# Kernel tuning notes

Hardware: AMD Instinct MI355X
Metric: run time of the kernel (lower is better)

The kernel has to match this reference:

```python
import jax, jax.numpy as jnp
import numpy as np

N, E = 50000, 640000
FEAT, EMB, HID, B = 128, 128, 512, 32


def setup_inputs() -> dict:
    key = jax.random.key(0)
    ks = jax.random.split(key, 12)
    def w(k, shape, fan_in):
        return jax.random.normal(k, shape, dtype=jnp.float32) / np.sqrt(fan_in)
    return {
        "x": jax.random.normal(ks[0], (N, FEAT), dtype=jnp.float32),
        "edge_index": jax.random.randint(ks[1], (2, E), 0, N, dtype=jnp.int64),
        "last_hidden": jax.random.normal(ks[2], (1, B, HID), dtype=jnp.float32),
        "W1_rel": w(ks[3], (FEAT, EMB), FEAT),
        "W1_root": w(ks[4], (FEAT, EMB), FEAT),
        "b1": jnp.zeros((EMB,), dtype=jnp.float32),
        "W2_rel": w(ks[5], (EMB, EMB), EMB),
        "W2_root": w(ks[6], (EMB, EMB), EMB),
        "b2": jnp.zeros((EMB,), dtype=jnp.float32),
        "Wp": w(ks[7], (HID, EMB), HID),
        "bp": jnp.zeros((EMB,), dtype=jnp.float32),
    }


def _rgcn(h, src, dst, W_rel, W_root, b):
    # transform-then-gather (N < E so cheaper): messages along edges src->dst
    msg = (h @ W_rel)[src]                                   # [E, emb]
    agg = jax.ops.segment_sum(msg, dst, num_segments=N)      # [N, emb]
    deg = jax.ops.segment_sum(jnp.ones((E,), h.dtype), dst, num_segments=N)
    agg = agg / jnp.maximum(deg, 1.0)[:, None]               # mean aggregation (PyG RGCNConv default)
    return agg + h @ W_root + b


def reference(x, edge_index, last_hidden, W1_rel, W1_root, b1, W2_rel, W2_root, b2, Wp, bp):
    src, dst = edge_index[0], edge_index[1]
    h = jax.nn.relu(_rgcn(x, src, dst, W1_rel, W1_root, b1))   # [N, emb]
    h = jax.nn.relu(_rgcn(h, src, dst, W2_rel, W2_root, b2))   # [N, emb]
    message_embed = (last_hidden @ Wp + bp)[0]                 # squeeze(0) -> [B, emb]
    scores = h @ message_embed.T                               # [N, B]
    return jax.nn.log_softmax(scores, axis=0)
```

## Files before the change

kernel.cpp:

```cpp
#include <hip/hip_runtime.h>
#include <hip/hip_bf16.h>

#define N_NODES 50000
#define N_EDGES 640000
#define DUMMY   N_NODES
#define CAP     56

typedef __attribute__((ext_vector_type(8))) short short8;
typedef __attribute__((ext_vector_type(4))) float floatx4;

__device__ __forceinline__ float bf2f(unsigned short u) {
    return __uint_as_float(((unsigned int)u) << 16);
}
__device__ __forceinline__ unsigned short f2bf(float x) {
    unsigned int u = __float_as_uint(x);
    u = (u + 0x7fffu + ((u >> 16) & 1u)) >> 16;
    return (unsigned short)u;
}
__device__ __forceinline__ unsigned char f2f8(float x) {
    int pk = __builtin_amdgcn_cvt_pk_fp8_f32(x, x, 0, false);
    return (unsigned char)(pk & 0xff);
}
__device__ __forceinline__ unsigned int pk4_fp8(float x0, float x1, float x2, float x3) {
    int v = __builtin_amdgcn_cvt_pk_fp8_f32(x0, x1, 0, false);
    v = __builtin_amdgcn_cvt_pk_fp8_f32(x2, x3, v, true);
    return (unsigned int)v;
}
__device__ __forceinline__ unsigned int pk2_bf16(float lo, float hi) {
    return (unsigned int)f2bf(lo) | ((unsigned int)f2bf(hi) << 16);
}

__global__ void __launch_bounds__(256) prep_k(const float* __restrict__ W0,
                                              const float* __restrict__ W1,
                                              const float* __restrict__ W2,
                                              const float* __restrict__ W3,
                                              unsigned short* __restrict__ T0,
                                              unsigned short* __restrict__ T1,
                                              unsigned short* __restrict__ T2,
                                              unsigned short* __restrict__ T3,
                                              int* __restrict__ cnt,
                                              const float* __restrict__ lh,
                                              const float* __restrict__ Wp,
                                              const float* __restrict__ bp,
                                              unsigned short* __restrict__ meb,
                                              unsigned short* __restrict__ ssrc,
                                              unsigned char* __restrict__ tbf,
                                              const int* __restrict__ src,
                                              const int* __restrict__ dst) {
    int b = blockIdx.x, tid = threadIdx.x;
    bool is_hist;
    int idx;
    if (b < 546) { is_hist = ((b & 1) == 0); idx = b >> 1; }
    else         { is_hist = true;            idx = 273 + (b - 546); }
    if (is_hist) {
        int e = idx * 256 + tid;
        int d = dst[e];
        int r = atomicAdd(&cnt[d], 1);
        if (r < CAP) ssrc[d * CAP + r] = (unsigned short)src[e];
        return;
    }
    int s = idx;
    if (s < 256) {
        int i2 = s * 256 + tid;
        int w = i2 >> 14;
        int r = i2 & 16383;
        int n = r >> 7, k = r & 127;
        const float* W = (w == 0) ? W0 : (w == 1) ? W1 : (w == 2) ? W2 : W3;
        unsigned short* T = (w == 0) ? T0 : (w == 1) ? T1 : (w == 2) ? T2 : T3;
        T[r] = f2bf(W[k * 128 + n]);
    } else if (s < 272) {
        int o = (s - 256) * 256 + tid;
        int i = o >> 7, c = o & 127;
        float acc = bp[c];
        const float4* lr = (const float4*)(lh + i * 512);
        #pragma unroll 4
        for (int k4 = 0; k4 < 128; k4++) {
            float4 v = lr[k4];
            acc += v.x * Wp[(4 * k4 + 0) * 128 + c] + v.y * Wp[(4 * k4 + 1) * 128 + c]
                 + v.z * Wp[(4 * k4 + 2) * 128 + c] + v.w * Wp[(4 * k4 + 3) * 128 + c];
        }
        meb[o] = f2bf(acc);
    } else {
        if (tid < 32) ((unsigned int*)(tbf + (size_t)DUMMY * 128))[tid] = 0;
    }
}

#define EPI_LD 132
template <bool AF32>
__device__ __forceinline__ void gemm_dual_lds32(int bid, int tid,
                                                const void* __restrict__ Ain,
                                                const unsigned short* __restrict__ BtRel,
                                                const unsigned short* __restrict__ BtRoot,
                                                unsigned char* __restrict__ Trel,
                                                unsigned short* __restrict__ Rootb,
                                                int M, char* __restrict__ pool) {
    int wid = tid >> 6, lane = tid & 63;
    int m = lane & 15, g = lane >> 4;
    int r0 = bid * 32;
    if constexpr (AF32) {
        const float* A = (const float*)Ain;
        #pragma unroll
        for (int j = 0; j < 2; j++) {
            int k = j * 256 + tid;
            int row = k >> 4;
            int grow = r0 + row; grow = (grow < M) ? grow : (M - 1);
            const float* p = A + (size_t)grow * 128 + (k & 15) * 8;
            float4 v0 = *(const float4*)p;
            float4 v1 = *(const float4*)(p + 4);
            short8 t8;
            t8[0] = (short)f2bf(v0.x); t8[1] = (short)f2bf(v0.y);
            t8[2] = (short)f2bf(v0.z); t8[3] = (short)f2bf(v0.w);
            t8[4] = (short)f2bf(v1.x); t8[5] = (short)f2bf(v1.y);
            t8[6] = (short)f2bf(v1.z); t8[7] = (short)f2bf(v1.w);
            *(short8*)(pool + ((k * 16) ^ ((row & 7) << 4))) = t8;
        }
    } else {
        const unsigned short* A = (const unsigned short*)Ain;
        #pragma unroll
        for (int j = 0; j < 2; j++) {
            int k = j * 256 + tid;
            int row = k >> 4;
            int grow = r0 + row; grow = (grow < M) ? grow : (M - 1);
            short8 v = *(const short8*)(A + (size_t)grow * 128 + (k & 15) * 8);
            *(short8*)(pool + ((k * 16) ^ ((row & 7) << 4))) = v;
        }
    }
    #pragma unroll
    for (int j = 0; j < 8; j++) {
        int k = j * 256 + tid;
        int row = k >> 4;
        short8 v = *(const short8*)(BtRel + (size_t)k * 8);
        *(short8*)(pool + 8192 + ((k * 16) ^ ((row & 7) << 4))) = v;
    }
    __syncthreads();
    int lrow = (wid >> 1) * 16 + m;
    int asw = (lrow & 7) << 4, abase = lrow * 256;
    short8 a[4];
    #pragma unroll
    for (int kt = 0; kt < 4; kt++)
        a[kt] = *(const short8*)(pool + ((abase + kt * 64 + g * 16) ^ asw));
    int browbase = (wid & 1) * 64;
    floatx4 accR[4], accO[4];
    #pragma unroll
    for (int ct = 0; ct < 4; ct++) {
        accR[ct] = (floatx4)(0.f);
        int brow = browbase + ct * 16 + m;
        int bbase = brow * 256, bsw = (brow & 7) << 4;
        #pragma unroll
        for (int kt = 0; kt < 4; kt++) {
            short8 bv = *(const short8*)(pool + 8192 + ((bbase + kt * 64 + g * 16) ^ bsw));
            accR[ct] = __builtin_amdgcn_mfma_f32_16x16x32_bf16(a[kt], bv, accR[ct], 0, 0, 0);
        }
    }
    __syncthreads();
    #pragma unroll
    for (int j = 0; j < 8; j++) {
        int k = j * 256 + tid;
        int row = k >> 4;
        short8 v = *(const short8*)(BtRoot + (size_t)k * 8);
        *(short8*)(pool + 8192 + ((k * 16) ^ ((row & 7) << 4))) = v;
    }
    __syncthreads();
    #pragma unroll
    for (int ct = 0; ct < 4; ct++) {
        accO[ct] = (floatx4)(0.f);
        int brow = browbase + ct * 16 + m;
        int bbase = brow * 256, bsw = (brow & 7) << 4;
        #pragma unroll
        for (int kt = 0; kt < 4; kt++) {
            short8 bv = *(const short8*)(pool + 8192 + ((bbase + kt * 64 + g * 16) ^ bsw));
            accO[ct] = __builtin_amdgcn_mfma_f32_16x16x32_bf16(a[kt], bv, accO[ct], 0, 0, 0);
        }
    }
    __syncthreads();
    float* epi = (float*)(pool + 8192);
    int rh = (wid >> 1) * 16, ch = (wid & 1) * 64;
    #pragma unroll
    for (int ct = 0; ct < 4; ct++)
        #pragma unroll
        for (int rg = 0; rg < 4; rg++)
            epi[(rh + g * 4 + rg) * EPI_LD + ch + ct * 16 + m] = accR[ct][rg];
    __syncthreads();
    {
        int lr = tid >> 3, c0 = (tid & 7) * 16;
        int ro = r0 + lr;
        const float* row = epi + lr * EPI_LD + c0;
        if (ro < M) {
            uint4 w;
            w.x = pk4_fp8(row[0],  row[1],  row[2],  row[3]);
            w.y = pk4_fp8(row[4],  row[5],  row[6],  row[7]);
            w.z = pk4_fp8(row[8],  row[9],  row[10], row[11]);
            w.w = pk4_fp8(row[12], row[13], row[14], row[15]);
            *(uint4*)(Trel + (size_t)ro * 128 + c0) = w;
        }
    }
    __syncthreads();
    #pragma unroll
    for (int ct = 0; ct < 4; ct++)
        #pragma unroll
        for (int rg = 0; rg < 4; rg++)
            epi[(rh + g * 4 + rg) * EPI_LD + ch + ct * 16 + m] = accO[ct][rg];
    __syncthreads();
    {
        int lr = tid >> 3, c0 = (tid & 7) * 16;
        int ro = r0 + lr;
        const float* row = epi + lr * EPI_LD + c0;
        if (ro < M) {
            uint4 w0, w1;
            w0.x = pk2_bf16(row[0],  row[1]);
            w0.y = pk2_bf16(row[2],  row[3]);
            w0.z = pk2_bf16(row[4],  row[5]);
            w0.w = pk2_bf16(row[6],  row[7]);
            w1.x = pk2_bf16(row[8],  row[9]);
            w1.y = pk2_bf16(row[10], row[11]);
            w1.z = pk2_bf16(row[12], row[13]);
            w1.w = pk2_bf16(row[14], row[15]);
            *(uint4*)(Rootb + (size_t)ro * 128 + c0) = w0;
            *(uint4*)(Rootb + (size_t)ro * 128 + c0 + 8) = w1;
        }
    }
}

__global__ void __launch_bounds__(256) gemm_f32_k(const float* __restrict__ A,
                                                  const unsigned short* __restrict__ BtRel,
                                                  const unsigned short* __restrict__ BtRoot,
                                                  unsigned char* __restrict__ Trel,
                                                  unsigned short* __restrict__ Rootb, int M) {
    __shared__ __align__(16) char pool[40960];
    gemm_dual_lds32<true>(blockIdx.x, threadIdx.x, A, BtRel, BtRoot, Trel, Rootb, M, pool);
}

__global__ void __launch_bounds__(256) gemm_dual_k(const unsigned short* __restrict__ A,
                                                   const unsigned short* __restrict__ BtRel,
                                                   const unsigned short* __restrict__ BtRoot,
                                                   unsigned char* __restrict__ Trel,
                                                   unsigned short* __restrict__ Rootb, int M) {
    __shared__ __align__(16) char pool[40960];
    gemm_dual_lds32<false>(blockIdx.x, threadIdx.x, A, BtRel, BtRoot, Trel, Rootb, M, pool);
}

__global__ void __launch_bounds__(256) agg_k(const int* __restrict__ cnt,
                                             const unsigned short* __restrict__ ssrc,
                                             const unsigned char* __restrict__ t,
                                             const unsigned short* __restrict__ rootb,
                                             const float* __restrict__ bias,
                                             unsigned short* __restrict__ hout) {
    int node = blockIdx.x * 4 + (threadIdx.x >> 6);
    if (node >= N_NODES) return;
    int lane = threadIdx.x & 63;
    int fl = lane & 31;
    int sh = (lane & 32) >> 1;
    int beg = node * CAP;
    int deg = cnt[node];
    deg = (deg < CAP) ? deg : CAP;
    int pad = (deg + 7) & ~7;
    const unsigned char* tf = t + fl * 4;
    float a0=0.f,a1=0.f,a2=0.f,a3=0.f;
    float b0=0.f,b1=0.f,b2=0.f,b3=0.f;
    int s0base = sh >> 4;
    for (int k = 0; k < pad; k += 16) {
        const unsigned short* sp = ssrc + beg + k;
        uint4 w0 = *(const uint4*)sp;
        uint4 w1 = (k + 8 < pad) ? *(const uint4*)(sp + 8) : make_uint4(0u, 0u, 0u, 0u);
        int s0 = k + s0base;
        int i0 = (s0 +  0 < deg) ? (int)((w0.x >> sh) & 0xffffu) : DUMMY;
        int i1 = (s0 +  2 < deg) ? (int)((w0.y >> sh) & 0xffffu) : DUMMY;
        int i2 = (s0 +  4 < deg) ? (int)((w0.z >> sh) & 0xffffu) : DUMMY;
        int i3 = (s0 +  6 < deg) ? (int)((w0.w >> sh) & 0xffffu) : DUMMY;
        int i4 = (s0 +  8 < deg) ? (int)((w1.x >> sh) & 0xffffu) : DUMMY;
        int i5 = (s0 + 10 < deg) ? (int)((w1.y >> sh) & 0xffffu) : DUMMY;
        int i6 = (s0 + 12 < deg) ? (int)((w1.z >> sh) & 0xffffu) : DUMMY;
        int i7 = (s0 + 14 < deg) ? (int)((w1.w >> sh) & 0xffffu) : DUMMY;
        unsigned int u0 = *(const unsigned int*)(tf + (size_t)i0 * 128);
        unsigned int u1 = *(const unsigned int*)(tf + (size_t)i1 * 128);
        unsigned int u2 = *(const unsigned int*)(tf + (size_t)i2 * 128);
        unsigned int u3 = *(const unsigned int*)(tf + (size_t)i3 * 128);
        unsigned int u4 = *(const unsigned int*)(tf + (size_t)i4 * 128);
        unsigned int u5 = *(const unsigned int*)(tf + (size_t)i5 * 128);
        unsigned int u6 = *(const unsigned int*)(tf + (size_t)i6 * 128);
        unsigned int u7 = *(const unsigned int*)(tf + (size_t)i7 * 128);
        a0 += __builtin_amdgcn_cvt_f32_fp8(u0, 0) + __builtin_amdgcn_cvt_f32_fp8(u1, 0);
        a1 += __builtin_amdgcn_cvt_f32_fp8(u0, 1) + __builtin_amdgcn_cvt_f32_fp8(u1, 1);
        a2 += __builtin_amdgcn_cvt_f32_fp8(u0, 2) + __builtin_amdgcn_cvt_f32_fp8(u1, 2);
        a3 += __builtin_amdgcn_cvt_f32_fp8(u0, 3) + __builtin_amdgcn_cvt_f32_fp8(u1, 3);
        b0 += __builtin_amdgcn_cvt_f32_fp8(u2, 0) + __builtin_amdgcn_cvt_f32_fp8(u3, 0);
        b1 += __builtin_amdgcn_cvt_f32_fp8(u2, 1) + __builtin_amdgcn_cvt_f32_fp8(u3, 1);
        b2 += __builtin_amdgcn_cvt_f32_fp8(u2, 2) + __builtin_amdgcn_cvt_f32_fp8(u3, 2);
        b3 += __builtin_amdgcn_cvt_f32_fp8(u2, 3) + __builtin_amdgcn_cvt_f32_fp8(u3, 3);
        a0 += __builtin_amdgcn_cvt_f32_fp8(u4, 0) + __builtin_amdgcn_cvt_f32_fp8(u5, 0);
        a1 += __builtin_amdgcn_cvt_f32_fp8(u4, 1) + __builtin_amdgcn_cvt_f32_fp8(u5, 1);
        a2 += __builtin_amdgcn_cvt_f32_fp8(u4, 2) + __builtin_amdgcn_cvt_f32_fp8(u5, 2);
        a3 += __builtin_amdgcn_cvt_f32_fp8(u4, 3) + __builtin_amdgcn_cvt_f32_fp8(u5, 3);
        b0 += __builtin_amdgcn_cvt_f32_fp8(u6, 0) + __builtin_amdgcn_cvt_f32_fp8(u7, 0);
        b1 += __builtin_amdgcn_cvt_f32_fp8(u6, 1) + __builtin_amdgcn_cvt_f32_fp8(u7, 1);
        b2 += __builtin_amdgcn_cvt_f32_fp8(u6, 2) + __builtin_amdgcn_cvt_f32_fp8(u7, 2);
        b3 += __builtin_amdgcn_cvt_f32_fp8(u6, 3) + __builtin_amdgcn_cvt_f32_fp8(u7, 3);
    }
    a0 += b0; a1 += b1; a2 += b2; a3 += b3;
    a0 += __shfl_xor(a0, 32);
    a1 += __shfl_xor(a1, 32);
    a2 += __shfl_xor(a2, 32);
    a3 += __shfl_xor(a3, 32);
    if ((lane & 32) == 0) {
        float inv = 1.f / fmaxf((float)deg, 1.f);
        int f = fl * 4;
        ushort4 r = *(const ushort4*)(rootb + (size_t)node * 128 + f);
        float4 bb = *(const float4*)(bias + f);
        ushort4 o;
        o.x = f2bf(fmaxf(a0 * inv + bf2f(r.x) + bb.x, 0.f));
        o.y = f2bf(fmaxf(a1 * inv + bf2f(r.y) + bb.y, 0.f));
        o.z = f2bf(fmaxf(a2 * inv + bf2f(r.z) + bb.z, 0.f));
        o.w = f2bf(fmaxf(a3 * inv + bf2f(r.w) + bb.w, 0.f));
        *(ushort4*)(hout + (size_t)node * 128 + f) = o;
    }
}

__global__ void __launch_bounds__(256) scores_cs_k(const unsigned short* __restrict__ A,
                                                   const unsigned short* __restrict__ Bt,
                                                   float* __restrict__ S,
                                                   float* __restrict__ pm,
                                                   float* __restrict__ ps) {
    __shared__ float Sl[64][33];
    __shared__ float sm[256], ss[256];
    int tid = threadIdx.x;
    int wid = tid >> 6, lane = tid & 63;
    int r0 = blockIdx.x * 64 + wid * 16;
    int m = lane & 15, g = lane >> 4;
    int row = r0 + m;
    int rowc = (row < N_NODES) ? row : (N_NODES - 1);
    short8 a[4];
    #pragma unroll
    for (int kt = 0; kt < 4; kt++)
        a[kt] = *(const short8*)(A + (size_t)rowc * 128 + kt * 32 + g * 8);
    floatx4 acc[2];
    acc[0] = (floatx4)(0.f);
    acc[1] = (floatx4)(0.f);
    #pragma unroll
    for (int ct = 0; ct < 2; ct++) {
        const unsigned short* b = Bt + (size_t)(ct * 16 + m) * 128 + g * 8;
        #pragma unroll
        for (int kt = 0; kt < 4; kt++) {
            short8 bv = *(const short8*)(b + kt * 32);
            acc[ct] = __builtin_amdgcn_mfma_f32_16x16x32_bf16(a[kt], bv, acc[ct], 0, 0, 0);
        }
    }
    #pragma unroll
    for (int ct = 0; ct < 2; ct++) {
        #pragma unroll
        for (int rg = 0; rg < 4; rg++) {
            int lr = wid * 16 + g * 4 + rg;
            int ro = r0 + g * 4 + rg;
            Sl[lr][ct * 16 + m] = acc[ct][rg];
            if (ro < N_NODES) S[(size_t)ro * 32 + ct * 16 + m] = acc[ct][rg];
        }
    }
    __syncthreads();
    int col = tid & 31, sub = tid >> 5;
    int blkbase = blockIdx.x * 64;
    float mm = -3.4e38f, s = 0.f;
    for (int r = sub; r < 64; r += 8) {
        if (blkbase + r < N_NODES) {
            float v = Sl[r][col];
            if (v > mm) { s = s * __expf(mm - v) + 1.f; mm = v; }
            else        { s += __expf(v - mm); }
        }
    }
    sm[tid] = mm; ss[tid] = s;
    __syncthreads();
    for (int off = 128; off >= 32; off >>= 1) {
        if (tid < off) {
            float m2 = sm[tid + off], s2 = ss[tid + off];
            float M = fmaxf(sm[tid], m2);
            ss[tid] = ss[tid] * __expf(sm[tid] - M) + s2 * __expf(m2 - M);
            sm[tid] = M;
        }
        __syncthreads();
    }
    if (tid < 32) { pm[tid * 782 + blockIdx.x] = sm[tid]; ps[tid * 782 + blockIdx.x] = ss[tid]; }
}

__global__ void __launch_bounds__(256) merge_k(const float* __restrict__ pm,
                                               const float* __restrict__ ps,
                                               float* __restrict__ cmg,
                                               float* __restrict__ clg) {
    __shared__ float sm[256], ss[256];
    int col = blockIdx.x;
    int t = threadIdx.x;
    float m = -3.4e38f, s = 0.f;
    for (int c = t; c < 782; c += 256) {
        float m2 = pm[col * 782 + c], s2 = ps[col * 782 + c];
        float M = fmaxf(m, m2);
        s = s * __expf(m - M) + s2 * __expf(m2 - M);
        m = M;
    }
    sm[t] = m; ss[t] = s;
    __syncthreads();
    for (int off = 128; off > 0; off >>= 1) {
        if (t < off) {
            float m2 = sm[t + off], s2 = ss[t + off];
            float M = fmaxf(sm[t], m2);
            ss[t] = ss[t] * __expf(sm[t] - M) + s2 * __expf(m2 - M);
            sm[t] = M;
        }
        __syncthreads();
    }
    if (t == 0) { cmg[col] = sm[0]; clg[col] = logf(ss[0]); }
}

__global__ void __launch_bounds__(256) final_k(const float* __restrict__ S,
                                               const float* __restrict__ cmg,
                                               const float* __restrict__ clg,
                                               float* __restrict__ out) {
    __shared__ float cc[32];
    int t = threadIdx.x;
    if (t < 32) cc[t] = cmg[t] + clg[t];
    __syncthreads();
    int idx = blockIdx.x * 256 + t;
    if (idx < N_NODES * 32) {
        int b = idx & 31;
        out[idx] = S[idx] - cc[b];
    }
}

extern "C" void kernel_launch(void* const* d_in, const int* in_sizes, int n_in,
                              void* d_out, int out_size, void* d_ws, size_t ws_size,
                              hipStream_t stream) {
    const float* x       = (const float*)d_in[0];
    const int*   ei      = (const int*)d_in[1];
    const float* lh      = (const float*)d_in[2];
    const float* W1_rel  = (const float*)d_in[3];
    const float* W1_root = (const float*)d_in[4];
    const float* b1      = (const float*)d_in[5];
    const float* W2_rel  = (const float*)d_in[6];
    const float* W2_root = (const float*)d_in[7];
    const float* b2      = (const float*)d_in[8];
    const float* Wp      = (const float*)d_in[9];
    const float* bp      = (const float*)d_in[10];
    float* out = (float*)d_out;
    float* ws  = (float*)d_ws;

    unsigned char*  tbf   = (unsigned char*)(ws + 3200000);
    unsigned short* rootb = (unsigned short*)(ws + 4800032);
    unsigned short* hb    = (unsigned short*)(ws + 8000032);
    unsigned short* Wt1r  = (unsigned short*)(ws + 11200032);
    unsigned short* Wt1o  = (unsigned short*)(ws + 11208224);
    unsigned short* Wt2r  = (unsigned short*)(ws + 11216416);
    unsigned short* Wt2o  = (unsigned short*)(ws + 11224608);
    unsigned short* MEb   = (unsigned short*)(ws + 11232800);
    float* pm   = ws + 11234848;
    float* ps   = ws + 11259872;
    float* cmg  = ws + 11284896;
    float* clg  = ws + 11284928;
    int*   cnt  = (int*)(ws + 11284960);
    float* S    = ws + 12519964;
    unsigned short* ssrc = (unsigned short*)(ws + 12519964);

    const int* srcp = ei;
    const int* dstp = ei + N_EDGES;

    const int ew_grid  = (N_NODES * 32 + 255) / 256;
    const int agg_grid = (N_NODES + 3) / 4;
    const int mm_grid  = (N_NODES + 63) / 64;
    const int g32_grid = (N_NODES + 31) / 32;

    hipMemsetAsync(cnt, 0, N_NODES * sizeof(int), stream);

    prep_k<<<2773, 256, 0, stream>>>(W1_rel, W1_root, W2_rel, W2_root,
                                     Wt1r, Wt1o, Wt2r, Wt2o,
                                     cnt, lh, Wp, bp, MEb, ssrc, tbf,
                                     srcp, dstp);

    gemm_f32_k<<<g32_grid, 256, 0, stream>>>(x, Wt1r, Wt1o, tbf, rootb, N_NODES);

    agg_k<<<agg_grid, 256, 0, stream>>>(cnt, ssrc, tbf, rootb, b1, hb);

    gemm_dual_k<<<g32_grid, 256, 0, stream>>>(hb, Wt2r, Wt2o, tbf, rootb, N_NODES);

    agg_k<<<agg_grid, 256, 0, stream>>>(cnt, ssrc, tbf, rootb, b2, hb);

    scores_cs_k<<<mm_grid, 256, 0, stream>>>(hb, MEb, S, pm, ps);

    merge_k<<<32, 256, 0, stream>>>(pm, ps, cmg, clg);

    final_k<<<ew_grid, 256, 0, stream>>>(S, cmg, clg, out);
}
```

Before: 218.2 us.

## Fuse edge histogram/bucketing into first-layer GEMM kernel via interleaved blocks

```diff
diff --git a/kernel.cpp b/kernel.cpp
--- a/kernel.cpp
+++ b/kernel.cpp
@@ -30,46 +30,30 @@
     return (unsigned int)f2bf(lo) | ((unsigned int)f2bf(hi) << 16);
 }
 
-__global__ void __launch_bounds__(256) prep_k(const float* __restrict__ W0,
-                                              const float* __restrict__ W1,
-                                              const float* __restrict__ W2,
-                                              const float* __restrict__ W3,
-                                              unsigned short* __restrict__ T0,
-                                              unsigned short* __restrict__ T1,
-                                              unsigned short* __restrict__ T2,
-                                              unsigned short* __restrict__ T3,
-                                              int* __restrict__ cnt,
-                                              const float* __restrict__ lh,
-                                              const float* __restrict__ Wp,
-                                              const float* __restrict__ bp,
-                                              unsigned short* __restrict__ meb,
-                                              unsigned short* __restrict__ ssrc,
-                                              unsigned char* __restrict__ tbf,
-                                              const int* __restrict__ src,
-                                              const int* __restrict__ dst) {
+__global__ void __launch_bounds__(256) prep0_k(const float* __restrict__ W0,
+                                               const float* __restrict__ W1,
+                                               const float* __restrict__ W2,
+                                               const float* __restrict__ W3,
+                                               unsigned short* __restrict__ T0,
+                                               unsigned short* __restrict__ T1,
+                                               unsigned short* __restrict__ T2,
+                                               unsigned short* __restrict__ T3,
+                                               const float* __restrict__ lh,
+                                               const float* __restrict__ Wp,
+                                               const float* __restrict__ bp,
+                                               unsigned short* __restrict__ meb,
+                                               unsigned char* __restrict__ tbf) {
     int b = blockIdx.x, tid = threadIdx.x;
-    bool is_hist;
-    int idx;
-    if (b < 546) { is_hist = ((b & 1) == 0); idx = b >> 1; }
-    else         { is_hist = true;            idx = 273 + (b - 546); }
-    if (is_hist) {
-        int e = idx * 256 + tid;
-        int d = dst[e];
-        int r = atomicAdd(&cnt[d], 1);
-        if (r < CAP) ssrc[d * CAP + r] = (unsigned short)src[e];
-        return;
-    }
-    int s = idx;
-    if (s < 256) {
-        int i2 = s * 256 + tid;
+    if (b < 256) {
+        int i2 = b * 256 + tid;
         int w = i2 >> 14;
         int r = i2 & 16383;
         int n = r >> 7, k = r & 127;
         const float* W = (w == 0) ? W0 : (w == 1) ? W1 : (w == 2) ? W2 : W3;
         unsigned short* T = (w == 0) ? T0 : (w == 1) ? T1 : (w == 2) ? T2 : T3;
         T[r] = f2bf(W[k * 128 + n]);
-    } else if (s < 272) {
-        int o = (s - 256) * 256 + tid;
+    } else if (b < 272) {
+        int o = (b - 256) * 256 + tid;
         int i = o >> 7, c = o & 127;
         float acc = bp[c];
         const float4* lr = (const float4*)(lh + i * 512);
@@ -221,13 +205,26 @@
     }
 }
 
-__global__ void __launch_bounds__(256) gemm_f32_k(const float* __restrict__ A,
+__global__ void __launch_bounds__(256) histgemm_k(int* __restrict__ cnt,
+                                                  const int* __restrict__ src,
+                                                  const int* __restrict__ dst,
+                                                  unsigned short* __restrict__ ssrc,
+                                                  const float* __restrict__ A,
                                                   const unsigned short* __restrict__ BtRel,
                                                   const unsigned short* __restrict__ BtRoot,
                                                   unsigned char* __restrict__ Trel,
-                                                  unsigned short* __restrict__ Rootb, int M) {
+                                                  unsigned short* __restrict__ Rootb) {
     __shared__ __align__(16) char pool[40960];
-    gemm_dual_lds32<true>(blockIdx.x, threadIdx.x, A, BtRel, BtRoot, Trel, Rootb, M, pool);
+    int b = blockIdx.x, tid = threadIdx.x;
+    if (b < 3126 && (b & 1)) {
+        gemm_dual_lds32<true>(b >> 1, tid, A, BtRel, BtRoot, Trel, Rootb, N_NODES, pool);
+        return;
+    }
+    int idx = (b < 3126) ? (b >> 1) : (1563 + (b - 3126));
+    int e = idx * 256 + tid;
+    int d = dst[e];
+    int r = atomicAdd(&cnt[d], 1);
+    if (r < CAP) ssrc[d * CAP + r] = (unsigned short)src[e];
 }
 
 __global__ void __launch_bounds__(256) gemm_dual_k(const unsigned short* __restrict__ A,
@@ -465,12 +462,12 @@
 
     hipMemsetAsync(cnt, 0, N_NODES * sizeof(int), stream);
 
-    prep_k<<<2773, 256, 0, stream>>>(W1_rel, W1_root, W2_rel, W2_root,
+    prep0_k<<<273, 256, 0, stream>>>(W1_rel, W1_root, W2_rel, W2_root,
                                      Wt1r, Wt1o, Wt2r, Wt2o,
-                                     cnt, lh, Wp, bp, MEb, ssrc, tbf,
-                                     srcp, dstp);
-
-    gemm_f32_k<<<g32_grid, 256, 0, stream>>>(x, Wt1r, Wt1o, tbf, rootb, N_NODES);
+                                     lh, Wp, bp, MEb, tbf);
+
+    histgemm_k<<<3126 + 937, 256, 0, stream>>>(cnt, srcp, dstp, ssrc,
+                                               x, Wt1r, Wt1o, tbf, rootb);
 
     agg_k<<<agg_grid, 256, 0, stream>>>(cnt, ssrc, tbf, rootb, b1, hb);
 
```

New measurement: 227.2 us. 1.04x slower.

## Build neighbor lists via bucketed counting sort instead of global atomics

Applied to the files above, without the earlier changes.

```diff
diff --git a/kernel.cpp b/kernel.cpp
--- a/kernel.cpp
+++ b/kernel.cpp
@@ -5,6 +5,8 @@
 #define N_EDGES 640000
 #define DUMMY   N_NODES
 #define CAP     56
+#define NBUCK   196
+#define EBLK    2500
 
 typedef __attribute__((ext_vector_type(8))) short short8;
 typedef __attribute__((ext_vector_type(4))) float floatx4;
@@ -38,25 +40,27 @@
                                               unsigned short* __restrict__ T1,
                                               unsigned short* __restrict__ T2,
                                               unsigned short* __restrict__ T3,
-                                              int* __restrict__ cnt,
                                               const float* __restrict__ lh,
                                               const float* __restrict__ Wp,
                                               const float* __restrict__ bp,
                                               unsigned short* __restrict__ meb,
-                                              unsigned short* __restrict__ ssrc,
                                               unsigned char* __restrict__ tbf,
-                                              const int* __restrict__ src,
-                                              const int* __restrict__ dst) {
+                                              const int* __restrict__ dst,
+                                              int* __restrict__ blockcnt) {
+    __shared__ int h[NBUCK];
     int b = blockIdx.x, tid = threadIdx.x;
     bool is_hist;
     int idx;
     if (b < 546) { is_hist = ((b & 1) == 0); idx = b >> 1; }
     else         { is_hist = true;            idx = 273 + (b - 546); }
     if (is_hist) {
+        if (tid < NBUCK) h[tid] = 0;
+        __syncthreads();
         int e = idx * 256 + tid;
-        int d = dst[e];
-        int r = atomicAdd(&cnt[d], 1);
-        if (r < CAP) ssrc[d * CAP + r] = (unsigned short)src[e];
+        int bk = (dst[e] >> 8) & 255;
+        if (bk < NBUCK) atomicAdd(&h[bk], 1);
+        __syncthreads();
+        if (tid < NBUCK) blockcnt[tid * EBLK + idx] = h[tid];
         return;
     }
     int s = idx;
@@ -85,6 +89,59 @@
     }
 }
 
+__global__ void __launch_bounds__(256) scan_k(int* __restrict__ blockcnt,
+                                              int* __restrict__ totals) {
+    __shared__ int sm[256];
+    int b = blockIdx.x, t = threadIdx.x;
+    int running = 0;
+    for (int c = 0; c < 10; c++) {
+        int i = c * 256 + t;
+        int v = (i < EBLK) ? blockcnt[b * EBLK + i] : 0;
+        sm[t] = v;
+        __syncthreads();
+        for (int off = 1; off < 256; off <<= 1) {
+            int u = (t >= off) ? sm[t - off] : 0;
+            __syncthreads();
+            sm[t] += u;
+            __syncthreads();
+        }
+        if (i < EBLK) blockcnt[b * EBLK + i] = running + sm[t] - v;
+        int ctot = sm[255];
+        __syncthreads();
+        running += ctot;
+    }
+    if (t == 0) totals[b] = running;
+}
+
+__global__ void __launch_bounds__(256) scatter_k(const int* __restrict__ src,
+                                                 const int* __restrict__ dst,
+                                                 const int* __restrict__ blockcnt,
+                                                 const int* __restrict__ totals,
+                                                 unsigned int* __restrict__ pairs) {
+    __shared__ int offl[NBUCK];
+    __shared__ int sm[256];
+    int blk = blockIdx.x, t = threadIdx.x;
+    int tv = (t < NBUCK) ? totals[t] : 0;
+    sm[t] = tv;
+    __syncthreads();
+    for (int off = 1; off < 256; off <<= 1) {
+        int u = (t >= off) ? sm[t - off] : 0;
+        __syncthreads();
+        sm[t] += u;
+        __syncthreads();
+    }
+    if (t < NBUCK) offl[t] = (sm[t] - tv) + blockcnt[t * EBLK + blk];
+    __syncthreads();
+    int e = blk * 256 + t;
+    int d = dst[e], s = src[e];
+    int bk = (d >> 8) & 255;
+    if (bk < NBUCK) {
+        int pos = atomicAdd(&offl[bk], 1);
+        if ((unsigned)pos < (unsigned)N_EDGES)
+            pairs[pos] = ((unsigned int)s << 16) | (unsigned int)(d & 0xffff);
+    }
+}
+
 #define EPI_LD 132
 template <bool AF32>
 __device__ __forceinline__ void gemm_dual_lds32(int bid, int tid,
@@ -221,13 +278,55 @@
     }
 }
 
-__global__ void __launch_bounds__(256) gemm_f32_k(const float* __restrict__ A,
-                                                  const unsigned short* __restrict__ BtRel,
-                                                  const unsigned short* __restrict__ BtRoot,
-                                                  unsigned char* __restrict__ Trel,
-                                                  unsigned short* __restrict__ Rootb, int M) {
+__global__ void __launch_bounds__(256) placegemm_k(const int* __restrict__ totals,
+                                                   const unsigned int* __restrict__ pairs,
+                                                   unsigned short* __restrict__ ssrc,
+                                                   int* __restrict__ cnt,
+                                                   const float* __restrict__ A,
+                                                   const unsigned short* __restrict__ BtRel,
+                                                   const unsigned short* __restrict__ BtRoot,
+                                                   unsigned char* __restrict__ Trel,
+                                                   unsigned short* __restrict__ Rootb) {
     __shared__ __align__(16) char pool[40960];
-    gemm_dual_lds32<true>(blockIdx.x, threadIdx.x, A, BtRel, BtRoot, Trel, Rootb, M, pool);
+    int t = threadIdx.x;
+    if (blockIdx.x >= NBUCK) {
+        gemm_dual_lds32<true>(blockIdx.x - NBUCK, t, A, BtRel, BtRoot,
+                              Trel, Rootb, N_NODES, pool);
+        return;
+    }
+    int b = blockIdx.x;
+    int* lcnt = (int*)pool;
+    int* sm   = (int*)(pool + 1024);
+    int* sb   = (int*)(pool + 2048);
+    int tv = (t < NBUCK) ? totals[t] : 0;
+    sm[t] = tv;
+    __syncthreads();
+    for (int off = 1; off < 256; off <<= 1) {
+        int u = (t >= off) ? sm[t - off] : 0;
+        __syncthreads();
+        sm[t] += u;
+        __syncthreads();
+    }
+    if (t == b) *sb = sm[t] - tv;
+    lcnt[t] = 0;
+    __syncthreads();
+    int base = *sb;
+    int n = totals[b];
+    if (n > N_EDGES) n = N_EDGES;
+    for (int i = t; i < n; i += 256) {
+        int gi = base + i;
+        if ((unsigned)gi >= (unsigned)N_EDGES) break;
+        unsigned int p = pairs[gi];
+        int dl = (int)(p & 0xffu);
+        int d = b * 256 + dl;
+        int s = (int)(p >> 16);
+        int r = atomicAdd(&lcnt[dl], 1);
+        if (d < N_NODES && r < CAP)
+            ssrc[(size_t)d * CAP + r] = (unsigned short)s;
+    }
+    __syncthreads();
+    int node = b * 256 + t;
+    if (node < N_NODES) cnt[node] = lcnt[t];
 }
 
 __global__ void __launch_bounds__(256) gemm_dual_k(const unsigned short* __restrict__ A,
@@ -452,6 +551,9 @@
     float* cmg  = ws + 11284896;
     float* clg  = ws + 11284928;
     int*   cnt  = (int*)(ws + 11284960);
+    int*   blockcnt = (int*)(ws + 11384964);
+    int*   totals   = (int*)(ws + 11874964);
+    unsigned int* pairs = (unsigned int*)(ws + 11875220);
     float* S    = ws + 12519964;
     unsigned short* ssrc = (unsigned short*)(ws + 12519964);
 
@@ -463,14 +565,16 @@
     const int mm_grid  = (N_NODES + 63) / 64;
     const int g32_grid = (N_NODES + 31) / 32;
 
-    hipMemsetAsync(cnt, 0, N_NODES * sizeof(int), stream);
-
     prep_k<<<2773, 256, 0, stream>>>(W1_rel, W1_root, W2_rel, W2_root,
                                      Wt1r, Wt1o, Wt2r, Wt2o,
-                                     cnt, lh, Wp, bp, MEb, ssrc, tbf,
-                                     srcp, dstp);
-
-    gemm_f32_k<<<g32_grid, 256, 0, stream>>>(x, Wt1r, Wt1o, tbf, rootb, N_NODES);
+                                     lh, Wp, bp, MEb, tbf, dstp, blockcnt);
+
+    scan_k<<<NBUCK, 256, 0, stream>>>(blockcnt, totals);
+
+    scatter_k<<<EBLK, 256, 0, stream>>>(srcp, dstp, blockcnt, totals, pairs);
+
+    placegemm_k<<<NBUCK + g32_grid, 256, 0, stream>>>(totals, pairs, ssrc, cnt,
+                                                      x, Wt1r, Wt1o, tbf, rootb);
 
     agg_k<<<agg_grid, 256, 0, stream>>>(cnt, ssrc, tbf, rootb, b1, hb);
 
```

After: 219.3 us. No clear change (+0.5%).
